# Kernel optimization log

Measured on AMD Instinct MI355X. Metric: run time of the kernel, lower is better.

## Reference

```python
import jax, jax.numpy as jnp
import numpy as np

B, C, H, W = 4, 64, 128, 128
O, K = 64, 3
STRIDE, PAD = 1, 1
K2 = K * K


def conv2d(x, w, b):
    out = jax.lax.conv_general_dilated(
        x, w, (STRIDE, STRIDE), [(PAD, PAD), (PAD, PAD)],
        dimension_numbers=('NCHW', 'OIHW', 'NCHW'))
    return out + b[None, :, None, None]


def setup_inputs() -> dict:
    key = jax.random.key(0)
    ks = jax.random.split(key, 6)
    return {
        'x': jax.random.normal(ks[0], (B, C, H, W), jnp.float32),
        'offset_w': jax.random.normal(ks[1], (2 * K2, C, K, K), jnp.float32) * 0.01,
        'offset_b': jax.random.normal(ks[2], (2 * K2,), jnp.float32) * 0.01,
        'mask_w': jax.random.normal(ks[3], (K2, C, K, K), jnp.float32) * 0.01,
        'mask_b': jnp.zeros((K2,), jnp.float32),
        'deform_w': jax.random.normal(ks[4], (O, C, K, K), jnp.float32) * (1.0 / np.sqrt(C * K2)),
        'deform_b': jax.random.normal(ks[5], (O,), jnp.float32) * 0.01,
    }


def _deform_conv(x, offset, mask, w, b):
    Bn, Cn, Hin, Win = x.shape
    Ho, Wo = offset.shape[2], offset.shape[3]
    off = offset.reshape(Bn, K2, 2, Ho, Wo)
    ky = jnp.repeat(jnp.arange(K), K)   # kernel row offset per location k
    kx = jnp.tile(jnp.arange(K), K)     # kernel col offset per location k
    yo = jnp.arange(Ho) * STRIDE - PAD
    xo = jnp.arange(Wo) * STRIDE - PAD
    # sampling positions [B,K2,Ho,Wo]
    py = off[:, :, 0] + ky[None, :, None, None] + yo[None, None, :, None]
    px = off[:, :, 1] + kx[None, :, None, None] + xo[None, None, None, :]
    y0 = jnp.floor(py)
    x0 = jnp.floor(px)
    wy1 = py - y0  # fractional weights
    wx1 = px - x0
    y0i = y0.astype(jnp.int32)
    x0i = x0.astype(jnp.int32)
    x_flat = x.reshape(Bn, Cn, Hin * Win)

    def corner(yi, xi, wgt):
        valid = (yi >= 0) & (yi < Hin) & (xi >= 0) & (xi < Win)
        yc = jnp.clip(yi, 0, Hin - 1)
        xc = jnp.clip(xi, 0, Win - 1)
        idx = (yc * Win + xc).reshape(Bn, -1)
        g = jnp.take_along_axis(x_flat, idx[:, None, :], axis=2)
        g = g.reshape(Bn, Cn, K2, Ho, Wo)
        return g * (wgt * valid)[:, None]

    val = (corner(y0i, x0i, (1 - wy1) * (1 - wx1))
           + corner(y0i, x0i + 1, (1 - wy1) * wx1)
           + corner(y0i + 1, x0i, wy1 * (1 - wx1))
           + corner(y0i + 1, x0i + 1, wy1 * wx1))
    val = val * mask[:, None]  # modulate, broadcast over channels
    out = jnp.einsum('bckhw,ock->bohw', val, w.reshape(w.shape[0], Cn, K2))
    return out + b[None, :, None, None]


def reference(x, offset_w, offset_b, mask_w, mask_b, deform_w, deform_b):
    offset = conv2d(x, offset_w, offset_b)
    mask = jax.nn.sigmoid(conv2d(x, mask_w, mask_b))
    return _deform_conv(x, offset, mask, deform_w, deform_b)
```

## Files before the change

### kernel.cpp

```cpp
#include <hip/hip_runtime.h>
#include <hip/hip_bf16.h>
#include <math.h>

#define BB 4
#define CC 64
#define HH 128
#define WW 128
#define HW 16384
#define CHW (CC*HW)

typedef __bf16 bf16;
typedef __attribute__((ext_vector_type(8))) __bf16 bf16x8;
typedef __attribute__((ext_vector_type(4))) __bf16 bf16x4;
typedef __attribute__((ext_vector_type(4))) float f32x4;
typedef __attribute__((ext_vector_type(4))) unsigned short u16x4;

#define MFMA(a, b, c) __builtin_amdgcn_mfma_f32_16x16x32_bf16((a), (b), (c), 0, 0, 0)

__global__ __launch_bounds__(256) void k_pre(const float* __restrict__ x,
        bf16* __restrict__ xt,
        const float* __restrict__ dw, const float* __restrict__ ow,
        const float* __restrict__ mw,
        bf16* __restrict__ wfd_hi,
        bf16* __restrict__ wfo_hi, bf16* __restrict__ wfo_lo) {
    __shared__ float tile[64][65];
    if (blockIdx.x < 1024) {
        int b  = blockIdx.x >> 8;
        int s0 = (blockIdx.x & 255) * 64;
        int t  = threadIdx.x;
        const float* xb = x + (size_t)b * CHW;
        int sl = (t & 15) * 4;
        int c0 = t >> 4;
        #pragma unroll
        for (int r = 0; r < 4; ++r) {
            int c = c0 + r * 16;
            float4 v = *(const float4*)&xb[(size_t)c * HW + s0 + sl];
            tile[c][sl]     = v.x;
            tile[c][sl + 1] = v.y;
            tile[c][sl + 2] = v.z;
            tile[c][sl + 3] = v.w;
        }
        __syncthreads();
        int lane = t & 63, w = t >> 6;
        int si = w * 16 + (lane >> 2);
        int cg = (lane & 3) * 16;
        bf16x8 h0, h1;
        #pragma unroll
        for (int j = 0; j < 8; ++j) {
            h0[j] = (bf16)tile[cg + j][si];
            h1[j] = (bf16)tile[cg + 8 + j][si];
        }
        bf16* dst = xt + (size_t)b * CHW + (size_t)(s0 + si) * 64 + cg;
        *(bf16x8*)dst       = h0;
        *(bf16x8*)(dst + 8) = h1;
    } else {
        int idx = (blockIdx.x - 1024) * 256 + threadIdx.x;
        if (idx < 36864) {
            int j    = idx & 7;
            int lane = (idx >> 3) & 63;
            int ks   = (idx >> 9) % 18;
            int nt   = idx / (512 * 18);
            int n    = nt * 16 + (lane & 15);
            int kglob = ks * 32 + (lane >> 4) * 8 + j;
            int kk = kglob >> 6, c = kglob & 63;
            wfd_hi[idx] = (bf16)dw[(n * 64 + c) * 9 + kk];
        } else {
            int idx2 = idx - 36864;
            int j    = idx2 & 7;
            int lane = (idx2 >> 3) & 63;
            int ks   = (idx2 >> 9) % 18;
            int nt   = idx2 / (512 * 18);
            int ch   = nt * 16 + (lane & 15);
            int kglob = ks * 32 + (lane >> 4) * 8 + j;
            int kk = kglob >> 6, c = kglob & 63;
            float w = 0.0f;
            if (ch < 18)      w = ow[(ch * 64 + c) * 9 + kk];
            else if (ch < 27) w = mw[((ch - 18) * 64 + c) * 9 + kk];
            bf16 h = (bf16)w;
            wfo_hi[idx2] = h;
            wfo_lo[idx2] = (bf16)(w - (float)h);
        }
    }
}

__global__ __launch_bounds__(256, 4) void k_fused(const bf16* __restrict__ xt,
        const bf16* __restrict__ wfo_hi, const bf16* __restrict__ wfo_lo,
        const bf16* __restrict__ wfd_hi,
        const float* __restrict__ ob, const float* __restrict__ mb,
        const float* __restrict__ db, float* __restrict__ out) {
    __shared__ float om_s[27 * 64];
    __shared__ __align__(8) bf16 sampw[576 * 4];
    __shared__ __align__(8) unsigned short sampo[576 * 4];

    int pos0 = blockIdx.x * 64;
    int wo0 = pos0 & 127;
    int ho  = (pos0 >> 7) & 127;
    int b   = pos0 >> 14;
    int t = threadIdx.x, wave = t >> 6, lane = t & 63;
    int m = lane & 15, g = lane >> 4;
    const bf16* xtb = xt + (size_t)b * CHW;

    {
        int st = wave;
        f32x4 acc0 = {0.f, 0.f, 0.f, 0.f};
        f32x4 acc1 = {0.f, 0.f, 0.f, 0.f};
        const bf16x8* bh0 = (const bf16x8*)wfo_hi + lane;
        const bf16x8* bl0 = (const bf16x8*)wfo_lo + lane;
        const bf16x8* bh1 = (const bf16x8*)wfo_hi + 18 * 64 + lane;
        const bf16x8* bl1 = (const bf16x8*)wfo_lo + 18 * 64 + lane;
        #pragma unroll
        for (int kk = 0; kk < 9; ++kk) {
            int y  = ho + kk / 3 - 1;
            int xx = wo0 + st * 16 + m + (kk % 3) - 1;
            bf16x8 ae = {};
            bf16x8 ao = {};
            if ((unsigned)y < 128u && (unsigned)xx < 128u) {
                const bf16* bp = xtb + ((size_t)(y * 128 + xx) << 6);
                ae = *(const bf16x8*)(bp + g * 8);
                ao = *(const bf16x8*)(bp + 32 + g * 8);
            }
            int ks0 = 2 * kk, ks1 = 2 * kk + 1;
            acc0 = MFMA(ae, bh0[ks0 * 64], acc0);
            acc0 = MFMA(ae, bl0[ks0 * 64], acc0);
            acc0 = MFMA(ao, bh0[ks1 * 64], acc0);
            acc0 = MFMA(ao, bl0[ks1 * 64], acc0);
            acc1 = MFMA(ae, bh1[ks0 * 64], acc1);
            acc1 = MFMA(ae, bl1[ks0 * 64], acc1);
            acc1 = MFMA(ao, bh1[ks1 * 64], acc1);
            acc1 = MFMA(ao, bl1[ks1 * 64], acc1);
        }
        int p64 = st * 16 + g * 4;
        float bias0 = ob[m];
        #pragma unroll
        for (int r = 0; r < 4; ++r)
            om_s[m * 64 + p64 + r] = acc0[r] + bias0;
        int ch1 = 16 + m;
        if (ch1 < 27) {
            float bias1 = (ch1 < 18) ? ob[ch1] : mb[ch1 - 18];
            #pragma unroll
            for (int r = 0; r < 4; ++r) {
                float v = acc1[r] + bias1;
                if (ch1 >= 18) v = 1.0f / (1.0f + __expf(-v));
                om_s[ch1 * 64 + p64 + r] = v;
            }
        }
    }
    __syncthreads();

    for (int task = t; task < 576; task += 256) {
        int p64 = task / 9, k = task - p64 * 9;
        float dy = om_s[(2 * k) * 64 + p64];
        float dx = om_s[(2 * k + 1) * 64 + p64];
        float mk = om_s[(18 + k) * 64 + p64];
        float py = (float)(ho - 1 + k / 3) + dy;
        float px = (float)(wo0 + p64 - 1 + (k % 3)) + dx;
        float y0f = floorf(py), x0f = floorf(px);
        float fy = py - y0f, fx = px - x0f;
        int y0 = (int)y0f, x0 = (int)x0f;
        int y1 = y0 + 1,  x1 = x0 + 1;
        bool vy0 = (unsigned)y0 < 128u, vy1 = (unsigned)y1 < 128u;
        bool vx0 = (unsigned)x0 < 128u, vx1 = (unsigned)x1 < 128u;
        int y0c = min(max(y0, 0), 127), y1c = min(max(y1, 0), 127);
        int x0c = min(max(x0, 0), 127), x1c = min(max(x1, 0), 127);
        bf16x4 wv;
        wv.x = (bf16)((vy0 && vx0) ? mk * (1.f - fy) * (1.f - fx) : 0.f);
        wv.y = (bf16)((vy0 && vx1) ? mk * (1.f - fy) * fx         : 0.f);
        wv.z = (bf16)((vy1 && vx0) ? mk * fy * (1.f - fx)         : 0.f);
        wv.w = (bf16)((vy1 && vx1) ? mk * fy * fx                 : 0.f);
        u16x4 ov;
        ov.x = (unsigned short)(y0c * 128 + x0c);
        ov.y = (unsigned short)(y0c * 128 + x1c);
        ov.z = (unsigned short)(y1c * 128 + x0c);
        ov.w = (unsigned short)(y1c * 128 + x1c);
        *(bf16x4*)&sampw[task * 4] = wv;
        *(u16x4*)&sampo[task * 4] = ov;
    }
    __syncthreads();

    {
        int st = wave;
        f32x4 acc[4];
        #pragma unroll
        for (int nt = 0; nt < 4; ++nt) acc[nt] = (f32x4){0.f, 0.f, 0.f, 0.f};
        const bf16x8* bhd = (const bf16x8*)wfd_hi + lane;
        int taskbase = (st * 16 + m) * 9;
        int cb0 = g * 8;
        int cb1 = 32 + g * 8;
        #pragma unroll
        for (int kk = 0; kk < 9; ++kk) {
            int task = taskbase + kk;
            bf16x4 wb = *(const bf16x4*)&sampw[task * 4];
            u16x4  o4 = *(const u16x4*)&sampo[task * 4];
            float w00 = (float)wb.x, w01 = (float)wb.y;
            float w10 = (float)wb.z, w11 = (float)wb.w;
            const bf16* p00 = xtb + ((int)o4.x << 6);
            const bf16* p01 = xtb + ((int)o4.y << 6);
            const bf16* p10 = xtb + ((int)o4.z << 6);
            const bf16* p11 = xtb + ((int)o4.w << 6);
            bf16x8 e00 = *(const bf16x8*)(p00 + cb0);
            bf16x8 e01 = *(const bf16x8*)(p01 + cb0);
            bf16x8 e10 = *(const bf16x8*)(p10 + cb0);
            bf16x8 e11 = *(const bf16x8*)(p11 + cb0);
            bf16x8 d00 = *(const bf16x8*)(p00 + cb1);
            bf16x8 d01 = *(const bf16x8*)(p01 + cb1);
            bf16x8 d10 = *(const bf16x8*)(p10 + cb1);
            bf16x8 d11 = *(const bf16x8*)(p11 + cb1);
            bf16x8 a0, a1;
            #pragma unroll
            for (int j = 0; j < 8; ++j) {
                float r0 = w00 * (float)e00[j] + w01 * (float)e01[j]
                         + w10 * (float)e10[j] + w11 * (float)e11[j];
                float r1 = w00 * (float)d00[j] + w01 * (float)d01[j]
                         + w10 * (float)d10[j] + w11 * (float)d11[j];
                a0[j] = (bf16)r0;
                a1[j] = (bf16)r1;
            }
            int ks0 = 2 * kk, ks1 = 2 * kk + 1;
            #pragma unroll
            for (int nt = 0; nt < 4; ++nt) {
                acc[nt] = MFMA(a0, bhd[(nt * 18 + ks0) * 64], acc[nt]);
                acc[nt] = MFMA(a1, bhd[(nt * 18 + ks1) * 64], acc[nt]);
            }
        }
        #pragma unroll
        for (int nt = 0; nt < 4; ++nt) {
            int o = nt * 16 + m;
            float bias = db[o];
            float4 vv = {acc[nt][0] + bias, acc[nt][1] + bias,
                         acc[nt][2] + bias, acc[nt][3] + bias};
            *(float4*)&out[((size_t)(b * 64 + o)) * HW + ho * 128 + wo0 + st * 16 + g * 4] = vv;
        }
    }
}

extern "C" void kernel_launch(void* const* d_in, const int* in_sizes, int n_in,
                              void* d_out, int out_size, void* d_ws, size_t ws_size,
                              hipStream_t stream) {
    const float* x   = (const float*)d_in[0];
    const float* ow  = (const float*)d_in[1];
    const float* ob  = (const float*)d_in[2];
    const float* mw  = (const float*)d_in[3];
    const float* mb  = (const float*)d_in[4];
    const float* dw  = (const float*)d_in[5];
    const float* db  = (const float*)d_in[6];
    float* out = (float*)d_out;

    bf16* xt = (bf16*)d_ws;
    bf16* wfd_hi = xt + (size_t)BB * HW * CC;
    bf16* wfo_hi = wfd_hi + 36864;
    bf16* wfo_lo = wfo_hi + 18432;

    k_pre<<<1024 + 216, 256, 0, stream>>>(x, xt, dw, ow, mw, wfd_hi, wfo_hi, wfo_lo);
    k_fused<<<(BB * HW) / 64, 256, 0, stream>>>(xt, wfo_hi, wfo_lo, wfd_hi, ob, mb, db, out);
}
```

Before: 140.2 us.

## Split fused kernel into offset/mask and deform kernels with LDS-staged gather

The fused kernel is split in two. The offset/mask conv writes bilinear sample weights and indices to global memory, and a separate deform kernel consumes them. In the deform kernel each lane gathers 4 channels (8 bytes) per corner for 4 sample points, rather than 8+8 channels for one point. The interpolated values are staged through a per-wave double-buffered LDS tile to form the MFMA A operand, which aims for better-coalesced gathers and lower register pressure in the deform phase. The cost is an extra kernel launch, a global round-trip for about 9 MB of sample data, and more LDS traffic.

```diff
diff --git a/kernel.cpp b/kernel.cpp
--- a/kernel.cpp
+++ b/kernel.cpp
@@ -83,14 +83,11 @@
     }
 }
 
-__global__ __launch_bounds__(256, 4) void k_fused(const bf16* __restrict__ xt,
+__global__ __launch_bounds__(256) void k_offmask(const bf16* __restrict__ xt,
         const bf16* __restrict__ wfo_hi, const bf16* __restrict__ wfo_lo,
-        const bf16* __restrict__ wfd_hi,
         const float* __restrict__ ob, const float* __restrict__ mb,
-        const float* __restrict__ db, float* __restrict__ out) {
+        bf16* __restrict__ sampw_g, unsigned short* __restrict__ sampo_g) {
     __shared__ float om_s[27 * 64];
-    __shared__ __align__(8) bf16 sampw[576 * 4];
-    __shared__ __align__(8) unsigned short sampo[576 * 4];
 
     int pos0 = blockIdx.x * 64;
     int wo0 = pos0 & 127;
@@ -147,8 +144,8 @@
     }
     __syncthreads();
 
-    for (int task = t; task < 576; task += 256) {
-        int p64 = task / 9, k = task - p64 * 9;
+    for (int tl = t; tl < 576; tl += 256) {
+        int p64 = tl / 9, k = tl - p64 * 9;
         float dy = om_s[(2 * k) * 64 + p64];
         float dx = om_s[(2 * k + 1) * 64 + p64];
         float mk = om_s[(18 + k) * 64 + p64];
@@ -172,64 +169,72 @@
         ov.y = (unsigned short)(y0c * 128 + x1c);
         ov.z = (unsigned short)(y1c * 128 + x0c);
         ov.w = (unsigned short)(y1c * 128 + x1c);
-        *(bf16x4*)&sampw[task * 4] = wv;
-        *(u16x4*)&sampo[task * 4] = ov;
-    }
-    __syncthreads();
-
-    {
-        int st = wave;
-        f32x4 acc[4];
-        #pragma unroll
-        for (int nt = 0; nt < 4; ++nt) acc[nt] = (f32x4){0.f, 0.f, 0.f, 0.f};
-        const bf16x8* bhd = (const bf16x8*)wfd_hi + lane;
-        int taskbase = (st * 16 + m) * 9;
-        int cb0 = g * 8;
-        int cb1 = 32 + g * 8;
-        #pragma unroll
-        for (int kk = 0; kk < 9; ++kk) {
-            int task = taskbase + kk;
-            bf16x4 wb = *(const bf16x4*)&sampw[task * 4];
-            u16x4  o4 = *(const u16x4*)&sampo[task * 4];
+        int gtask = pos0 * 9 + tl;
+        *(bf16x4*)&sampw_g[gtask * 4] = wv;
+        *(u16x4*)&sampo_g[gtask * 4] = ov;
+    }
+}
+
+__global__ __launch_bounds__(256, 4) void k_deform(const bf16* __restrict__ xt,
+        const bf16* __restrict__ wfd_hi,
+        const bf16* __restrict__ sampw_g, const unsigned short* __restrict__ sampo_g,
+        const float* __restrict__ db, float* __restrict__ out) {
+    __shared__ __align__(16) char stage[4 * 2 * 16 * 144];
+
+    int t = threadIdx.x, wave = t >> 6, lane = t & 63;
+    int m = lane & 15, g = lane >> 4;
+    int p16  = blockIdx.x * 4 + wave;
+    int pos0 = p16 * 16;
+    int wo0 = pos0 & 127;
+    int ho  = (pos0 >> 7) & 127;
+    int b   = pos0 >> 14;
+    const bf16* xtb = xt + (size_t)b * CHW;
+    char* mybuf = stage + wave * (2 * 16 * 144);
+
+    f32x4 acc[4];
+    #pragma unroll
+    for (int nt = 0; nt < 4; ++nt) acc[nt] = (f32x4){0.f, 0.f, 0.f, 0.f};
+    const bf16x8* bhd = (const bf16x8*)wfd_hi + lane;
+    int cq8 = m * 8;
+
+    for (int kk = 0; kk < 9; ++kk) {
+        char* buf = mybuf + (kk & 1) * (16 * 144);
+        #pragma unroll
+        for (int it = 0; it < 4; ++it) {
+            int s = it * 4 + g;
+            int gtask = (pos0 + s) * 9 + kk;
+            bf16x4 wb = *(const bf16x4*)&sampw_g[gtask * 4];
+            u16x4  o4 = *(const u16x4*)&sampo_g[gtask * 4];
+            bf16x4 c0 = *(const bf16x4*)(xtb + ((int)o4.x << 6) + m * 4);
+            bf16x4 c1 = *(const bf16x4*)(xtb + ((int)o4.y << 6) + m * 4);
+            bf16x4 c2 = *(const bf16x4*)(xtb + ((int)o4.z << 6) + m * 4);
+            bf16x4 c3 = *(const bf16x4*)(xtb + ((int)o4.w << 6) + m * 4);
             float w00 = (float)wb.x, w01 = (float)wb.y;
             float w10 = (float)wb.z, w11 = (float)wb.w;
-            const bf16* p00 = xtb + ((int)o4.x << 6);
-            const bf16* p01 = xtb + ((int)o4.y << 6);
-            const bf16* p10 = xtb + ((int)o4.z << 6);
-            const bf16* p11 = xtb + ((int)o4.w << 6);
-            bf16x8 e00 = *(const bf16x8*)(p00 + cb0);
-            bf16x8 e01 = *(const bf16x8*)(p01 + cb0);
-            bf16x8 e10 = *(const bf16x8*)(p10 + cb0);
-            bf16x8 e11 = *(const bf16x8*)(p11 + cb0);
-            bf16x8 d00 = *(const bf16x8*)(p00 + cb1);
-            bf16x8 d01 = *(const bf16x8*)(p01 + cb1);
-            bf16x8 d10 = *(const bf16x8*)(p10 + cb1);
-            bf16x8 d11 = *(const bf16x8*)(p11 + cb1);
-            bf16x8 a0, a1;
-            #pragma unroll
-            for (int j = 0; j < 8; ++j) {
-                float r0 = w00 * (float)e00[j] + w01 * (float)e01[j]
-                         + w10 * (float)e10[j] + w11 * (float)e11[j];
-                float r1 = w00 * (float)d00[j] + w01 * (float)d01[j]
-                         + w10 * (float)d10[j] + w11 * (float)d11[j];
-                a0[j] = (bf16)r0;
-                a1[j] = (bf16)r1;
-            }
-            int ks0 = 2 * kk, ks1 = 2 * kk + 1;
-            #pragma unroll
-            for (int nt = 0; nt < 4; ++nt) {
-                acc[nt] = MFMA(a0, bhd[(nt * 18 + ks0) * 64], acc[nt]);
-                acc[nt] = MFMA(a1, bhd[(nt * 18 + ks1) * 64], acc[nt]);
-            }
-        }
+            float r0 = w00 * (float)c0.x + w01 * (float)c1.x + w10 * (float)c2.x + w11 * (float)c3.x;
+            float r1 = w00 * (float)c0.y + w01 * (float)c1.y + w10 * (float)c2.y + w11 * (float)c3.y;
+            float r2 = w00 * (float)c0.z + w01 * (float)c1.z + w10 * (float)c2.z + w11 * (float)c3.z;
+            float r3 = w00 * (float)c0.w + w01 * (float)c1.w + w10 * (float)c2.w + w11 * (float)c3.w;
+            bf16x4 hv = {(bf16)r0, (bf16)r1, (bf16)r2, (bf16)r3};
+            *(bf16x4*)(buf + s * 144 + cq8) = hv;
+        }
+        bf16x8 a0 = *(const bf16x8*)(buf + m * 144 + g * 16);
+        bf16x8 a1 = *(const bf16x8*)(buf + m * 144 + 64 + g * 16);
+        int ks0 = 2 * kk, ks1 = ks0 + 1;
         #pragma unroll
         for (int nt = 0; nt < 4; ++nt) {
-            int o = nt * 16 + m;
-            float bias = db[o];
-            float4 vv = {acc[nt][0] + bias, acc[nt][1] + bias,
-                         acc[nt][2] + bias, acc[nt][3] + bias};
-            *(float4*)&out[((size_t)(b * 64 + o)) * HW + ho * 128 + wo0 + st * 16 + g * 4] = vv;
-        }
+            acc[nt] = MFMA(a0, bhd[(nt * 18 + ks0) * 64], acc[nt]);
+            acc[nt] = MFMA(a1, bhd[(nt * 18 + ks1) * 64], acc[nt]);
+        }
+    }
+
+    #pragma unroll
+    for (int nt = 0; nt < 4; ++nt) {
+        int o = nt * 16 + m;
+        float bias = db[o];
+        float4 vv = {acc[nt][0] + bias, acc[nt][1] + bias,
+                     acc[nt][2] + bias, acc[nt][3] + bias};
+        *(float4*)&out[((size_t)(b * 64 + o)) * HW + ho * 128 + wo0 + g * 4] = vv;
     }
 }
 
@@ -245,11 +250,14 @@
     const float* db  = (const float*)d_in[6];
     float* out = (float*)d_out;
 
-    bf16* xt = (bf16*)d_ws;
-    bf16* wfd_hi = xt + (size_t)BB * HW * CC;
-    bf16* wfo_hi = wfd_hi + 36864;
-    bf16* wfo_lo = wfo_hi + 18432;
+    bf16* xt      = (bf16*)d_ws;
+    bf16* wfd_hi  = xt + (size_t)BB * HW * CC;
+    bf16* wfo_hi  = wfd_hi + 36864;
+    bf16* wfo_lo  = wfo_hi + 18432;
+    bf16* sampw_g = wfo_lo + 18432;
+    unsigned short* sampo_g = (unsigned short*)(sampw_g + (size_t)589824 * 4);
 
     k_pre<<<1024 + 216, 256, 0, stream>>>(x, xt, dw, ow, mw, wfd_hi, wfo_hi, wfo_lo);
-    k_fused<<<(BB * HW) / 64, 256, 0, stream>>>(xt, wfo_hi, wfo_lo, wfd_hi, ob, mb, db, out);
-}
+    k_offmask<<<(BB * HW) / 64, 256, 0, stream>>>(xt, wfo_hi, wfo_lo, ob, mb, sampw_g, sampo_g);
+    k_deform<<<(BB * HW) / 64, 256, 0, stream>>>(xt, wfd_hi, sampw_g, sampo_g, db, out);
+}
```

Measured after the change: 140.4 us. Within noise of the previous version (+0.2%).
